# Performance work log

Measured on AMD Instinct MI355X. Metric: run time of the kernel, lower is better.

The kernel has to match this reference:

```python
import jax, jax.numpy as jnp
import numpy as np

B, NQ, NK, C, OUT = 4, 2048, 2048, 4, 64
H = 16          # hidden size of the radial MLP (hardcoded in MlpRBF)
WINDOW = 0.25   # window_size default in MlpRBF


def setup_inputs() -> dict:
    key = jax.random.key(0)
    ks = jax.random.split(key, 20)
    s = 0.5
    return {
        "key_pos": jax.random.uniform(ks[0], (B, NK, 1), dtype=jnp.float32),
        "queries": jax.random.uniform(ks[1], (B, NQ, 1), dtype=jnp.float32),
        "values": jax.random.normal(ks[2], (B, NK, 1), dtype=jnp.float32),
        "key_chan": jax.random.randint(ks[3], (B, NK), 0, C),
        # radial MLP: 1 -> 16 -> 16 -> 16 -> 1, ReLU hidden activations
        "w0": jax.random.normal(ks[4], (H, 1)) * s, "b0": jax.random.normal(ks[5], (H,)) * 0.1,
        "w1": jax.random.normal(ks[6], (H, H)) * (s / np.sqrt(H)), "b1": jax.random.normal(ks[7], (H,)) * 0.1,
        "w2": jax.random.normal(ks[8], (H, H)) * (s / np.sqrt(H)), "b2": jax.random.normal(ks[9], (H,)) * 0.1,
        "w3": jax.random.normal(ks[10], (1, H)) * (s / np.sqrt(H)), "b3": jax.random.normal(ks[11], (1,)) * 0.1,
        # density_transform: Linear(1,1)
        "wd": jax.random.normal(ks[12], (1, 1)) * s, "bd": jax.random.normal(ks[13], (1,)) * 0.1,
        # resizer: Linear(2*C, OUT)
        "wr": jax.random.normal(ks[14], (OUT, 2 * C)) * (s / np.sqrt(2 * C)), "br": jax.random.normal(ks[15], (OUT,)) * 0.1,
    }


def reference(key_pos, queries, values, key_chan,
              w0, b0, w1, b1, w2, b2, w3, b3, wd, bd, wr, br):
    # pairwise |key - query| distances: [B, NQ, NK] (is_abs_dist=True)
    diff = jnp.abs(key_pos[:, None, :, 0] - queries[:, :, None, 0])
    window = diff < WINDOW                              # [B, NQ, NK] bool

    # per-pair radial MLP (x_dim=1 input, 3 hidden layers of 16, scalar out)
    x = diff[..., None]                                 # [B, NQ, NK, 1]
    h = jax.nn.relu(x @ w0.T + b0)
    h = jax.nn.relu(h @ w1.T + b1)
    h = jax.nn.relu(h @ w2.T + b2)
    raw = (h @ w3.T + b3)[..., 0]                       # [B, NQ, NK]
    weight = jnp.abs(raw) * window.astype(raw.dtype)    # mask_and_apply + abs + window mask

    # per-channel masked reduction (equivalent to gathering keys of each channel)
    onehot = jax.nn.one_hot(key_chan, C, dtype=weight.dtype)      # [B, NK, C]
    density = jnp.einsum('bqk,bkc->bqc', weight, onehot)          # [B, NQ, C]
    numer = jnp.einsum('bqk,bkc->bqc', weight, onehot * values)   # values: [B, NK, 1]
    targets = numer / (density + 1e-5)                            # normalized weighted sum

    # density channel: sigmoid(Linear(density*0.1 - 1))
    dens_feat = jax.nn.sigmoid((density * 0.1 - 1.0) * wd[0, 0] + bd[0])

    # per-channel SetConv output is cat([target, density]) -> interleave: [t0,d0,t1,d1,...]
    feat = jnp.stack([targets, dens_feat], axis=-1).reshape(targets.shape[0], targets.shape[1], 2 * C)
    return feat @ wr.T + br                             # [B, NQ, OUT]
```

## Files before the change

### kernel.cpp

```cpp
#include <hip/hip_runtime.h>
#include <math.h>

constexpr int B_  = 4;
constexpr int NQ_ = 2048;
constexpr int NK_ = 2048;
constexpr int C_  = 4;
constexpr int OUT_ = 64;
constexpr int H_  = 16;
constexpr float WINDOW_ = 0.25f;

constexpr int   TAB_   = 4096;
constexpr float SCALE_ = TAB_ / WINDOW_;
constexpr int   QW_    = 4;
constexpr int   SLOT_  = 1024;
constexpr int   NBIN_  = 64;
constexpr float SENT_  = 4e9f;

constexpr size_t OFF_TAB  = 0;
constexpr size_t OFF_SORT = 16384;
constexpr size_t OFF_BINS = 16384 + 16 * SLOT_ * 8;

__global__ __launch_bounds__(256) void preprocess(
    const float* __restrict__ key_pos,
    const float* __restrict__ values,
    const int*   __restrict__ key_chan,
    const float* __restrict__ w0, const float* __restrict__ b0,
    const float* __restrict__ w1, const float* __restrict__ b1,
    const float* __restrict__ w2, const float* __restrict__ b2,
    const float* __restrict__ w3, const float* __restrict__ b3,
    float* __restrict__ tab,
    float2* __restrict__ sorted,
    int*    __restrict__ bins)
{
    const int tid = threadIdx.x;

    if (blockIdx.x < 16) {
        const int i = blockIdx.x * 256 + tid;
        const float x = ((float)i + 0.5f) * (1.0f / SCALE_);
        float h[H_], g[H_];
        #pragma unroll
        for (int j = 0; j < H_; ++j)
            h[j] = fmaxf(fmaf(x, w0[j], b0[j]), 0.f);
        #pragma unroll
        for (int j = 0; j < H_; ++j) {
            float a = b1[j];
            #pragma unroll
            for (int k = 0; k < H_; ++k) a = fmaf(w1[j * H_ + k], h[k], a);
            g[j] = fmaxf(a, 0.f);
        }
        #pragma unroll
        for (int j = 0; j < H_; ++j) {
            float a = b2[j];
            #pragma unroll
            for (int k = 0; k < H_; ++k) a = fmaf(w2[j * H_ + k], g[k], a);
            h[j] = fmaxf(a, 0.f);
        }
        float a = b3[0];
        #pragma unroll
        for (int k = 0; k < H_; ++k) a = fmaf(w3[k], h[k], a);
        tab[i] = fabsf(a);
        return;
    }

    const int slot = blockIdx.x - 16;
    const int b    = slot >> 2;
    const int c    = slot & 3;

    __shared__ int   hist[NBIN_ + 1];
    __shared__ int   ofs [NBIN_];
    __shared__ float lpos[SLOT_];
    __shared__ float lval[SLOT_];

    if (tid <= NBIN_) hist[tid] = 0;
    __syncthreads();

    const float* kp = key_pos  + b * NK_;
    const float* vv = values   + b * NK_;
    const int*   cc = key_chan + b * NK_;

    for (int i = tid; i < NK_; i += 256) {
        if (cc[i] == c) {
            const int bin = min((int)(kp[i] * (float)NBIN_), NBIN_ - 1);
            atomicAdd(&hist[bin], 1);
        }
    }
    __syncthreads();

    if (tid == 0) {
        int run = 0;
        #pragma unroll
        for (int t = 0; t < NBIN_; ++t) {
            const int h = hist[t];
            hist[t] = run; ofs[t] = run; run += h;
        }
        hist[NBIN_] = run;
    }
    __syncthreads();

    const int cnt = hist[NBIN_];
    if (tid <= NBIN_) bins[slot * (NBIN_ + 1) + tid] = hist[tid];

    for (int i = tid; i < NK_; i += 256) {
        if (cc[i] == c) {
            const float p   = kp[i];
            const int   bin = min((int)(p * (float)NBIN_), NBIN_ - 1);
            const int   idx = atomicAdd(&ofs[bin], 1);
            lpos[idx] = p; lval[idx] = vv[i];
        }
    }
    __syncthreads();

    for (int i = tid; i < SLOT_; i += 256)
        sorted[slot * SLOT_ + i] =
            (i < cnt) ? make_float2(lpos[i], lval[i]) : make_float2(SENT_, 0.f);
}

__global__ __launch_bounds__(256, 8) void setconv_main(
    const float*  __restrict__ queries,
    const float2* __restrict__ sorted,
    const int*    __restrict__ bins,
    const float*  __restrict__ tab,
    const float*  __restrict__ wd, const float* __restrict__ bd,
    const float*  __restrict__ wr, const float* __restrict__ br,
    float* __restrict__ out)
{
    __shared__ __align__(16) float ltab[TAB_];

    const int tid = threadIdx.x;

    {
        const float4* t4 = (const float4*)tab;
        float4*       l4 = (float4*)ltab;
        #pragma unroll
        for (int i = 0; i < TAB_ / 4 / 256; ++i)
            l4[i * 256 + tid] = t4[i * 256 + tid];
    }
    __syncthreads();

    const int blk  = blockIdx.x;
    const int b    = blk >> 9;
    const int tile = blk & 511;
    const int wave = tid >> 6;
    const int lane = tid & 63;

    const int   qi   = tile * QW_ + wave;
    const float qpos = queries[b * NQ_ + qi];

    int lo_bin = (int)floorf((qpos - WINDOW_) * (float)NBIN_);
    lo_bin = (lo_bin < 0) ? 0 : ((lo_bin > NBIN_) ? NBIN_ : lo_bin);
    int hi_bin = (int)ceilf((qpos + WINDOW_) * (float)NBIN_);
    hi_bin = (hi_bin < 0) ? 0 : ((hi_bin > NBIN_) ? NBIN_ : hi_bin);

    int k[4];
    const float2* seg[4];
    int rounds = 0;
    #pragma unroll
    for (int c = 0; c < 4; ++c) {
        const int slot = b * 4 + c;
        const int* bs  = bins + slot * (NBIN_ + 1);
        k[c] = bs[lo_bin];
        const int span = bs[hi_bin] - k[c];
        const int rc   = (span + 63) >> 6;
        rounds = (rc > rounds) ? rc : rounds;
        seg[c] = sorted + slot * SLOT_;
    }

    float dens[4] = {0.f, 0.f, 0.f, 0.f};
    float num [4] = {0.f, 0.f, 0.f, 0.f};

    float2 cur[4];
    #pragma unroll
    for (int c = 0; c < 4; ++c)
        cur[c] = seg[c][min(k[c], SLOT_ - 64) + lane];

    for (int r = 0; r < rounds; ++r) {
        float2 nxt[4];
        #pragma unroll
        for (int c = 0; c < 4; ++c)
            nxt[c] = seg[c][min(k[c] + 64, SLOT_ - 64) + lane];

        #pragma unroll
        for (int c = 0; c < 4; ++c) {
            const float dd = fabsf(cur[c].x - qpos);
            const float t  = fminf(dd * SCALE_, (float)(TAB_ - 1));
            const float tv = ltab[(int)t];
            const float w  = (dd < WINDOW_) ? tv : 0.f;
            dens[c] += w;
            num [c]  = fmaf(w, cur[c].y, num[c]);
        }

        #pragma unroll
        for (int c = 0; c < 4; ++c) { cur[c] = nxt[c]; k[c] += 64; }
    }

    #pragma unroll
    for (int off = 32; off >= 1; off >>= 1) {
        #pragma unroll
        for (int c = 0; c < 4; ++c) {
            dens[c] += __shfl_xor(dens[c], off, 64);
            num [c] += __shfl_xor(num [c], off, 64);
        }
    }

    const float wd0 = wd[0];
    const float bd0 = bd[0];
    float wrow[8];
    #pragma unroll
    for (int j = 0; j < 8; ++j) wrow[j] = wr[lane * 8 + j];
    float acc = br[lane];

    #pragma unroll
    for (int c = 0; c < 4; ++c) {
        const float tgt = num[c] / (dens[c] + 1e-5f);
        const float x   = (dens[c] * 0.1f - 1.0f) * wd0 + bd0;
        const float df  = 1.0f / (1.0f + expf(-x));
        acc = fmaf(wrow[2 * c],     tgt, acc);
        acc = fmaf(wrow[2 * c + 1], df,  acc);
    }
    out[(b * NQ_ + qi) * OUT_ + lane] = acc;
}

extern "C" void kernel_launch(void* const* d_in, const int* in_sizes, int n_in,
                              void* d_out, int out_size, void* d_ws, size_t ws_size,
                              hipStream_t stream) {
    (void)in_sizes; (void)n_in; (void)out_size; (void)ws_size;

    char* ws = (char*)d_ws;
    float*  tab    = (float*) (ws + OFF_TAB);
    float2* sorted = (float2*)(ws + OFF_SORT);
    int*    bins   = (int*)   (ws + OFF_BINS);

    preprocess<<<dim3(32), dim3(256), 0, stream>>>(
        (const float*)d_in[0],
        (const float*)d_in[2],
        (const int*)  d_in[3],
        (const float*)d_in[4],  (const float*)d_in[5],
        (const float*)d_in[6],  (const float*)d_in[7],
        (const float*)d_in[8],  (const float*)d_in[9],
        (const float*)d_in[10], (const float*)d_in[11],
        tab, sorted, bins);

    setconv_main<<<dim3(B_ * (NQ_ / QW_)), dim3(256), 0, stream>>>(
        (const float*)d_in[1],
        sorted, bins, tab,
        (const float*)d_in[12], (const float*)d_in[13],
        (const float*)d_in[14], (const float*)d_in[15],
        (float*)d_out);
}
```

Before: 101.4 us.

## Split wave into per-channel 16-lane groups and register-cache preprocess keys

The main kernel now gives each of the four channels its own 16-lane group within a wave. Each group walks only its channel's window in 16-wide steps, instead of every lane visiting all four channels in 64-wide steps bounded by the largest span. This cuts wasted lanes and masked iterations caused by rounding each channel's span up to 64. The reduction becomes a 16-lane butterfly plus cross-group shuffles, and channels are resolved per lane via an xor index. The preprocess kernel loads key channel, position, value and bin into registers once, reusing them for both the histogram and scatter passes instead of reading global memory twice.

```diff
diff --git a/kernel.cpp b/kernel.cpp
--- a/kernel.cpp
+++ b/kernel.cpp
@@ -72,18 +72,24 @@
     __shared__ float lval[SLOT_];
 
     if (tid <= NBIN_) hist[tid] = 0;
-    __syncthreads();
 
     const float* kp = key_pos  + b * NK_;
     const float* vv = values   + b * NK_;
     const int*   cc = key_chan + b * NK_;
 
-    for (int i = tid; i < NK_; i += 256) {
-        if (cc[i] == c) {
-            const int bin = min((int)(kp[i] * (float)NBIN_), NBIN_ - 1);
-            atomicAdd(&hist[bin], 1);
-        }
-    }
+    constexpr int EPT = NK_ / 256;
+    int   ch[EPT]; float p[EPT]; float v[EPT]; int bn[EPT];
+    #pragma unroll
+    for (int t = 0; t < EPT; ++t) {
+        const int i = t * 256 + tid;
+        ch[t] = cc[i]; p[t] = kp[i]; v[t] = vv[i];
+        bn[t] = min((int)(p[t] * (float)NBIN_), NBIN_ - 1);
+    }
+    __syncthreads();
+
+    #pragma unroll
+    for (int t = 0; t < EPT; ++t)
+        if (ch[t] == c) atomicAdd(&hist[bn[t]], 1);
     __syncthreads();
 
     if (tid == 0) {
@@ -100,12 +106,11 @@
     const int cnt = hist[NBIN_];
     if (tid <= NBIN_) bins[slot * (NBIN_ + 1) + tid] = hist[tid];
 
-    for (int i = tid; i < NK_; i += 256) {
-        if (cc[i] == c) {
-            const float p   = kp[i];
-            const int   bin = min((int)(p * (float)NBIN_), NBIN_ - 1);
-            const int   idx = atomicAdd(&ofs[bin], 1);
-            lpos[idx] = p; lval[idx] = vv[i];
+    #pragma unroll
+    for (int t = 0; t < EPT; ++t) {
+        if (ch[t] == c) {
+            const int idx = atomicAdd(&ofs[bn[t]], 1);
+            lpos[idx] = p[t]; lval[idx] = v[t];
         }
     }
     __syncthreads();
@@ -142,6 +147,8 @@
     const int tile = blk & 511;
     const int wave = tid >> 6;
     const int lane = tid & 63;
+    const int g    = lane >> 4;
+    const int l16  = lane & 15;
 
     const int   qi   = tile * QW_ + wave;
     const float qpos = queries[b * NQ_ + qi];
@@ -151,71 +158,56 @@
     int hi_bin = (int)ceilf((qpos + WINDOW_) * (float)NBIN_);
     hi_bin = (hi_bin < 0) ? 0 : ((hi_bin > NBIN_) ? NBIN_ : hi_bin);
 
-    int k[4];
-    const float2* seg[4];
-    int rounds = 0;
-    #pragma unroll
-    for (int c = 0; c < 4; ++c) {
-        const int slot = b * 4 + c;
-        const int* bs  = bins + slot * (NBIN_ + 1);
-        k[c] = bs[lo_bin];
-        const int span = bs[hi_bin] - k[c];
-        const int rc   = (span + 63) >> 6;
-        rounds = (rc > rounds) ? rc : rounds;
-        seg[c] = sorted + slot * SLOT_;
-    }
-
-    float dens[4] = {0.f, 0.f, 0.f, 0.f};
-    float num [4] = {0.f, 0.f, 0.f, 0.f};
-
-    float2 cur[4];
-    #pragma unroll
-    for (int c = 0; c < 4; ++c)
-        cur[c] = seg[c][min(k[c], SLOT_ - 64) + lane];
+    const int slot = b * 4 + g;
+    const int* bs  = bins + slot * (NBIN_ + 1);
+    const int k0   = bs[lo_bin];
+    const int span = bs[hi_bin] - k0;
+    const float2* seg = sorted + slot * SLOT_;
+
+    int rounds = (span + 15) >> 4;
+    rounds = max(rounds, __shfl_xor(rounds, 16, 64));
+    rounds = max(rounds, __shfl_xor(rounds, 32, 64));
+
+    float d = 0.f, n = 0.f;
+
+    float2 cur = seg[min(k0, SLOT_ - 16) + l16];
 
     for (int r = 0; r < rounds; ++r) {
-        float2 nxt[4];
-        #pragma unroll
-        for (int c = 0; c < 4; ++c)
-            nxt[c] = seg[c][min(k[c] + 64, SLOT_ - 64) + lane];
-
-        #pragma unroll
-        for (int c = 0; c < 4; ++c) {
-            const float dd = fabsf(cur[c].x - qpos);
-            const float t  = fminf(dd * SCALE_, (float)(TAB_ - 1));
-            const float tv = ltab[(int)t];
-            const float w  = (dd < WINDOW_) ? tv : 0.f;
-            dens[c] += w;
-            num [c]  = fmaf(w, cur[c].y, num[c]);
-        }
-
-        #pragma unroll
-        for (int c = 0; c < 4; ++c) { cur[c] = nxt[c]; k[c] += 64; }
-    }
-
-    #pragma unroll
-    for (int off = 32; off >= 1; off >>= 1) {
-        #pragma unroll
-        for (int c = 0; c < 4; ++c) {
-            dens[c] += __shfl_xor(dens[c], off, 64);
-            num [c] += __shfl_xor(num [c], off, 64);
-        }
-    }
+        const float2 nxt = seg[min(k0 + ((r + 1) << 4), SLOT_ - 16) + l16];
+
+        const float dd = fabsf(cur.x - qpos);
+        const float t  = fminf(dd * SCALE_, (float)(TAB_ - 1));
+        const float tv = ltab[(int)t];
+        const float w  = (dd < WINDOW_) ? tv : 0.f;
+        d += w;
+        n  = fmaf(w, cur.y, n);
+
+        cur = nxt;
+    }
+
+    #pragma unroll
+    for (int off = 8; off >= 1; off >>= 1) {
+        d += __shfl_xor(d, off, 64);
+        n += __shfl_xor(n, off, 64);
+    }
+    float Dv[4], Nv[4];
+    Dv[0] = d;                      Nv[0] = n;
+    Dv[1] = __shfl_xor(d, 16, 64);  Nv[1] = __shfl_xor(n, 16, 64);
+    Dv[2] = __shfl_xor(d, 32, 64);  Nv[2] = __shfl_xor(n, 32, 64);
+    Dv[3] = __shfl_xor(d, 48, 64);  Nv[3] = __shfl_xor(n, 48, 64);
 
     const float wd0 = wd[0];
     const float bd0 = bd[0];
-    float wrow[8];
-    #pragma unroll
-    for (int j = 0; j < 8; ++j) wrow[j] = wr[lane * 8 + j];
     float acc = br[lane];
 
     #pragma unroll
-    for (int c = 0; c < 4; ++c) {
-        const float tgt = num[c] / (dens[c] + 1e-5f);
-        const float x   = (dens[c] * 0.1f - 1.0f) * wd0 + bd0;
+    for (int m = 0; m < 4; ++m) {
+        const int   c   = g ^ m;
+        const float tgt = Nv[m] / (Dv[m] + 1e-5f);
+        const float x   = (Dv[m] * 0.1f - 1.0f) * wd0 + bd0;
         const float df  = 1.0f / (1.0f + expf(-x));
-        acc = fmaf(wrow[2 * c],     tgt, acc);
-        acc = fmaf(wrow[2 * c + 1], df,  acc);
+        acc = fmaf(wr[lane * 8 + 2 * c],     tgt, acc);
+        acc = fmaf(wr[lane * 8 + 2 * c + 1], df,  acc);
     }
     out[(b * NQ_ + qi) * OUT_ + lane] = acc;
 }
```

After: 99.15 us. -2.2%, faster.
